# Optimization experiments

Hardware: AMD Instinct MI355X
Metric: run time of the kernel (lower is better)

The kernel has to match this reference:

```python
import jax, jax.numpy as jnp
import numpy as np

N, E, B = 50000, 500000, 64
IN_DIM, HID, H, NC = 128, 32, 8, 10
SLOPE = 0.2  # DGL GATConv leaky_relu negative_slope default


def setup_inputs() -> dict:
    key = jax.random.key(0)
    ks = jax.random.split(key, 14)
    feat = jax.random.normal(ks[0], (N, IN_DIM), dtype=jnp.float32)
    src = jax.random.randint(ks[1], (E,), 0, N, dtype=jnp.int32)
    dst = jax.random.randint(ks[2], (E,), 0, N, dtype=jnp.int32)
    node2graph = jnp.sort(jax.random.randint(ks[3], (N,), 0, B, dtype=jnp.int32))
    s1 = 1.0 / np.sqrt(IN_DIM)
    s2 = 1.0 / np.sqrt(H * HID)
    W1 = jax.random.normal(ks[4], (IN_DIM, H * HID), dtype=jnp.float32) * s1
    al1 = jax.random.normal(ks[5], (H, HID), dtype=jnp.float32) * 0.1
    ar1 = jax.random.normal(ks[6], (H, HID), dtype=jnp.float32) * 0.1
    b1 = jnp.zeros((H * HID,), dtype=jnp.float32)
    W2 = jax.random.normal(ks[7], (H * HID, H * HID), dtype=jnp.float32) * s2
    al2 = jax.random.normal(ks[8], (H, HID), dtype=jnp.float32) * 0.1
    ar2 = jax.random.normal(ks[9], (H, HID), dtype=jnp.float32) * 0.1
    b2 = jnp.zeros((H * HID,), dtype=jnp.float32)
    Wc = jax.random.normal(ks[10], (H * HID, NC), dtype=jnp.float32) * s2
    bc = jnp.zeros((NC,), dtype=jnp.float32)
    return dict(feat=feat, src=src, dst=dst, node2graph=node2graph,
                W1=W1, al1=al1, ar1=ar1, b1=b1,
                W2=W2, al2=al2, ar2=ar2, b2=b2, Wc=Wc, bc=bc)


def gat_layer(h, src, dst, W, al, ar, b):
    # h: [N, F_in] -> out: [N, H, HID]   (DGL GATConv math, no dropout)
    fs = (h @ W).reshape(N, H, HID)                      # projected src/dst feats
    el = jnp.sum(fs * al[None], axis=-1)                 # [N, H]
    er = jnp.sum(fs * ar[None], axis=-1)                 # [N, H]
    e = jax.nn.leaky_relu(el[src] + er[dst], SLOPE)      # [E, H] per-edge logits
    # edge softmax over incoming edges of each dst node (numerically stable)
    emax = jax.ops.segment_max(e, dst, num_segments=N)   # [N, H]
    ex = jnp.exp(e - emax[dst])                          # [E, H]
    denom = jax.ops.segment_sum(ex, dst, num_segments=N) # [N, H]
    alpha = ex / denom[dst]                              # [E, H]
    msg = alpha[:, :, None] * fs[src]                    # [E, H, HID]
    rst = jax.ops.segment_sum(msg, dst, num_segments=N)  # [N, H, HID]
    return rst + b.reshape(1, H, HID)


def reference(feat, src, dst, node2graph, W1, al1, ar1, b1, W2, al2, ar2, b2, Wc, bc):
    h = jax.nn.relu(gat_layer(feat, src, dst, W1, al1, ar1, b1)).reshape(N, H * HID)
    h = gat_layer(h, src, dst, W2, al2, ar2, b2).reshape(N, H * HID)
    # dgl.mean_nodes: per-graph mean over nodes of the batched graph
    counts = jax.ops.segment_sum(jnp.ones((N,), dtype=h.dtype), node2graph, num_segments=B)
    hg = jax.ops.segment_sum(h, node2graph, num_segments=B) / jnp.maximum(counts, 1.0)[:, None]
    return hg @ Wc + bc  # [B, NC]
```

## Files before the change

kernel.cpp:

```cpp
#include <hip/hip_runtime.h>
#include <hip/hip_bf16.h>

#define N_NODES 50000
#define N_EDGES 500000
#define N_GRAPHS 64
#define FDIM 256
#define NHEAD 8
#define NC 10
#define SLOPE 0.2f
#define MPAD 50048
#define NBKT 196
#define CNTN (NBKT * 256)
#define SCAN_NB (CNTN / 1024)
#define NB1 256
#define EPB 1956
#define LDSW 40
#define PSPLIT 16

typedef __attribute__((ext_vector_type(8))) short bf16x8;
typedef __attribute__((ext_vector_type(4))) float f32x4;
typedef __attribute__((ext_vector_type(2))) float f32x2;
typedef __attribute__((ext_vector_type(4))) unsigned u32x4;

__device__ __forceinline__ unsigned short f2bf(float f) {
  unsigned x = __float_as_uint(f);
  x += 0x7fff + ((x >> 16) & 1);
  return (unsigned short)(x >> 16);
}
__device__ __forceinline__ float b2f(unsigned short u) {
  return __uint_as_float((unsigned)u << 16);
}
__device__ __forceinline__ int fswz(int node, int off) {
  return off ^ ((node & 7) << 5) ^ (((node >> 3) & 1) << 4);
}

__global__ void cast_gstart_kernel(const float* __restrict__ W1, const float* __restrict__ W2,
                                   unsigned short* __restrict__ Wt1, unsigned short* __restrict__ Wt2,
                                   const int* __restrict__ n2g, int* __restrict__ gstart) {
  int e = blockIdx.x * blockDim.x + threadIdx.x;
  if (e < 256 * 128) {
    int n = e / 128, k = e % 128;
    Wt1[(size_t)n * 128 + k] = f2bf(W1[(size_t)k * 256 + n]);
  } else if (e < 256 * 128 + 256 * 256) {
    int t2 = e - 256 * 128;
    int n = t2 / 256, k = t2 % 256;
    Wt2[(size_t)n * 256 + k] = f2bf(W2[(size_t)k * 256 + n]);
  } else {
    int i = e - (256 * 128 + 256 * 256);
    if (i < N_NODES) {
      int g1 = n2g[i];
      int g0 = (i == 0) ? -1 : n2g[i - 1];
      for (int g = g0 + 1; g <= g1; ++g) gstart[g] = i;
      if (i == N_NODES - 1) {
        for (int g = g1 + 1; g <= N_GRAPHS; ++g) gstart[g] = N_NODES;
      }
    }
  }
}

__global__ void bucket_hist_kernel(const int* __restrict__ dst, int* __restrict__ counts) {
  __shared__ int hist[NBKT];
  int t = threadIdx.x, b = blockIdx.x;
  if (t < NBKT) hist[t] = 0;
  __syncthreads();
  int start = b * EPB;
  int end = min(start + EPB, N_EDGES);
  for (int base = start + t * 4; base < end; base += 1024) {
    if (base + 3 < end) {
      int4 d = *(const int4*)(dst + base);
      atomicAdd(&hist[d.x >> 8], 1); atomicAdd(&hist[d.y >> 8], 1);
      atomicAdd(&hist[d.z >> 8], 1); atomicAdd(&hist[d.w >> 8], 1);
    } else {
      for (int e2 = base; e2 < end; ++e2) atomicAdd(&hist[dst[e2] >> 8], 1);
    }
  }
  __syncthreads();
  if (t < NBKT) counts[t * NB1 + b] = hist[t];
}

__global__ void scan_local_kernel(const int* __restrict__ deg, int* __restrict__ outv,
                                  int* __restrict__ bsum, int n) {
  __shared__ int ws[4];
  int t = threadIdx.x, lane = t & 63, w = t >> 6;
  int base = blockIdx.x * 1024 + t * 4;
  int4 v = make_int4(0, 0, 0, 0);
  if (base + 3 < n) {
    v = *(const int4*)(deg + base);
  } else {
    if (base + 0 < n) v.x = deg[base + 0];
    if (base + 1 < n) v.y = deg[base + 1];
    if (base + 2 < n) v.z = deg[base + 2];
    if (base + 3 < n) v.w = deg[base + 3];
  }
  int s = v.x + v.y + v.z + v.w;
  int x = s;
  #pragma unroll
  for (int off = 1; off < 64; off <<= 1) {
    int y = __shfl_up(x, off);
    if (lane >= off) x += y;
  }
  if (lane == 63) ws[w] = x;
  __syncthreads();
  int woff = 0;
  #pragma unroll
  for (int i = 0; i < 4; ++i) woff += (i < w) ? ws[i] : 0;
  int excl = woff + x - s;
  int4 o;
  o.x = excl;
  o.y = excl + v.x;
  o.z = excl + v.x + v.y;
  o.w = excl + v.x + v.y + v.z;
  if (base + 3 < n) {
    *(int4*)(outv + base) = o;
  } else {
    if (base + 0 < n) outv[base + 0] = o.x;
    if (base + 1 < n) outv[base + 1] = o.y;
    if (base + 2 < n) outv[base + 2] = o.z;
    if (base + 3 < n) outv[base + 3] = o.w;
  }
  if (t == 255) bsum[blockIdx.x] = woff + x;
}

__global__ void scan_add_kernel(int* __restrict__ cbase, const int* __restrict__ bsum,
                                int* __restrict__ rowstart, int n) {
  __shared__ int boff[64];
  int t = threadIdx.x;
  if (t < 64) {
    int v = (t < SCAN_NB) ? bsum[t] : 0;
    int x = v;
    #pragma unroll
    for (int off = 1; off < 64; off <<= 1) {
      int y = __shfl_up(x, off);
      if (t >= off) x += y;
    }
    boff[t] = x - v;
  }
  __syncthreads();
  int i = blockIdx.x * blockDim.x + threadIdx.x;
  if (i < n) cbase[i] += boff[i >> 10];
  if (i == 0) rowstart[N_NODES] = N_EDGES;
}

__global__ void bucket_scatter_kernel(const int* __restrict__ src, const int* __restrict__ dst,
                                      const int* __restrict__ cbase, int2* __restrict__ ebuf) {
  __shared__ int cur[NBKT];
  int t = threadIdx.x, b = blockIdx.x;
  if (t < NBKT) cur[t] = 0;
  __syncthreads();
  int start = b * EPB;
  int end = min(start + EPB, N_EDGES);
  for (int base = start + t * 4; base < end; base += 1024) {
    if (base + 3 < end) {
      int4 s = *(const int4*)(src + base);
      int4 d = *(const int4*)(dst + base);
      int bk, r;
      bk = d.x >> 8; r = atomicAdd(&cur[bk], 1); ebuf[cbase[bk * NB1 + b] + r] = make_int2(s.x, d.x);
      bk = d.y >> 8; r = atomicAdd(&cur[bk], 1); ebuf[cbase[bk * NB1 + b] + r] = make_int2(s.y, d.y);
      bk = d.z >> 8; r = atomicAdd(&cur[bk], 1); ebuf[cbase[bk * NB1 + b] + r] = make_int2(s.z, d.z);
      bk = d.w >> 8; r = atomicAdd(&cur[bk], 1); ebuf[cbase[bk * NB1 + b] + r] = make_int2(s.w, d.w);
    } else {
      for (int e2 = base; e2 < end; ++e2) {
        int dd = dst[e2];
        int bk = dd >> 8;
        int r = atomicAdd(&cur[bk], 1);
        ebuf[cbase[bk * NB1 + b] + r] = make_int2(src[e2], dd);
      }
    }
  }
}

__global__ void csr_bucket_kernel(const int2* __restrict__ ebuf, const int* __restrict__ cbase,
                                  int* __restrict__ rowstart, int* __restrict__ esrc) {
  __shared__ int hist[256];
  __shared__ int cur[256];
  __shared__ int ws[4];
  int t = threadIdx.x;
  int bkt = blockIdx.x;
  int segstart = cbase[bkt * NB1];
  int segend = (bkt + 1 < NBKT) ? cbase[(bkt + 1) * NB1] : N_EDGES;
  hist[t] = 0;
  __syncthreads();
  for (int e = segstart + t; e < segend; e += 256)
    atomicAdd(&hist[ebuf[e].y & 255], 1);
  __syncthreads();
  int lane = t & 63, w = t >> 6;
  int v = hist[t], x = v;
  #pragma unroll
  for (int off = 1; off < 64; off <<= 1) {
    int y = __shfl_up(x, off);
    if (lane >= off) x += y;
  }
  if (lane == 63) ws[w] = x;
  __syncthreads();
  int woff = 0;
  #pragma unroll
  for (int i = 0; i < 4; ++i) woff += (i < w) ? ws[i] : 0;
  int excl = woff + x - v;
  cur[t] = excl;
  int node = bkt * 256 + t;
  if (node < N_NODES) rowstart[node] = segstart + excl;
  __syncthreads();
  for (int e = segstart + t; e < segend; e += 256) {
    int2 p = ebuf[e];
    int r = atomicAdd(&cur[p.y & 255], 1);
    esrc[segstart + r] = p.x;
  }
}

template<int K, bool AF32>
__global__ void gemm_mfma(const void* __restrict__ Avoid,
                          const unsigned short* __restrict__ Wt,
                          unsigned char* __restrict__ fs,
                          const float* __restrict__ al, const float* __restrict__ ar,
                          float* __restrict__ el, float* __restrict__ er, int nrows) {
  constexpr int KC = K / 32;
  __shared__ __align__(16) unsigned short LDSbuf[(64 + 256) * LDSW];
  unsigned short* Albs = LDSbuf;
  unsigned short* Wlds = LDSbuf + 64 * LDSW;
  const float* Af = (const float*)Avoid;
  const unsigned short* Ab = (const unsigned short*)Avoid;
  int t = threadIdx.x;
  int lane = t & 63;
  int w = t >> 6;
  int row0 = blockIdx.x * 64;
  int m = lane & 15;
  int q = lane >> 4;
  float4 a32[2];
  bf16x8 a16;
  bf16x8 wtr[4];
  int arow = t >> 2, apiece = t & 3;
  int agrow = min(row0 + arow, nrows - 1);
  int frow0 = t >> 3, fquad0 = t & 7;
  int frow1 = (256 + t) >> 3, fquad1 = t & 7;
  int fgrow0 = min(row0 + frow0, nrows - 1);
  int fgrow1 = min(row0 + frow1, nrows - 1);

  auto stage = [&](int kc) {
    if (AF32) {
      a32[0] = *(const float4*)(Af + (size_t)fgrow0 * K + kc * 32 + fquad0 * 4);
      a32[1] = *(const float4*)(Af + (size_t)fgrow1 * K + kc * 32 + fquad1 * 4);
    } else {
      a16 = *(const bf16x8*)(Ab + (size_t)agrow * K + kc * 32 + apiece * 8);
    }
    #pragma unroll
    for (int j = 0; j < 4; ++j) {
      int row = j * 64 + (t >> 2);
      wtr[j] = *(const bf16x8*)(Wt + (size_t)row * K + kc * 32 + (t & 3) * 8);
    }
  };
  auto commit = [&]() {
    if (AF32) {
      ushort4 o0, o1;
      o0.x = f2bf(a32[0].x); o0.y = f2bf(a32[0].y); o0.z = f2bf(a32[0].z); o0.w = f2bf(a32[0].w);
      o1.x = f2bf(a32[1].x); o1.y = f2bf(a32[1].y); o1.z = f2bf(a32[1].z); o1.w = f2bf(a32[1].w);
      *(ushort4*)(Albs + frow0 * LDSW + fquad0 * 4) = o0;
      *(ushort4*)(Albs + frow1 * LDSW + fquad1 * 4) = o1;
    } else {
      *(bf16x8*)(Albs + arow * LDSW + apiece * 8) = a16;
    }
    #pragma unroll
    for (int j = 0; j < 4; ++j) {
      int row = j * 64 + (t >> 2);
      *(bf16x8*)(Wlds + row * LDSW + (t & 3) * 8) = wtr[j];
    }
  };

  f32x4 acc[16];
  #pragma unroll
  for (int nt = 0; nt < 16; ++nt) acc[nt] = (f32x4){0.f, 0.f, 0.f, 0.f};

  stage(0);
  commit();
  for (int kc = 0; kc < KC; ++kc) {
    __syncthreads();
    if (kc + 1 < KC) stage(kc + 1);
    bf16x8 af = *(const bf16x8*)(Albs + (w * 16 + m) * LDSW + q * 8);
    #pragma unroll
    for (int nt = 0; nt < 16; ++nt) {
      bf16x8 bfv = *(const bf16x8*)(Wlds + (nt * 16 + m) * LDSW + q * 8);
      acc[nt] = __builtin_amdgcn_mfma_f32_16x16x32_bf16(bfv, af, acc[nt], 0, 0, 0);
    }
    __syncthreads();
    if (kc + 1 < KC) commit();
  }
  unsigned char* fsst = (unsigned char*)LDSbuf;
  float* elst = (float*)(fsst + 16384);
  float* erst = elst + 512;

  int nloc = w * 16 + m;
  float elh[NHEAD], erh[NHEAD];
  #pragma unroll
  for (int h = 0; h < NHEAD; ++h) { elh[h] = 0.f; erh[h] = 0.f; }
  #pragma unroll
  for (int nt = 0; nt < 16; ++nt) {
    int h = nt >> 1;
    int c0 = (nt & 1) * 16 + q * 4;
    float4 a4 = *(const float4*)(al + h * 32 + c0);
    float4 r4 = *(const float4*)(ar + h * 32 + c0);
    elh[h] += acc[nt][0] * a4.x + acc[nt][1] * a4.y + acc[nt][2] * a4.z + acc[nt][3] * a4.w;
    erh[h] += acc[nt][0] * r4.x + acc[nt][1] * r4.y + acc[nt][2] * r4.z + acc[nt][3] * r4.w;
  }
  #pragma unroll
  for (int h = 0; h < NHEAD; ++h) {
    elh[h] += __shfl_xor(elh[h], 16); elh[h] += __shfl_xor(elh[h], 32);
    erh[h] += __shfl_xor(erh[h], 16); erh[h] += __shfl_xor(erh[h], 32);
  }
  #pragma unroll
  for (int nt = 0; nt < 16; ++nt) {
    int pk = 0;
    pk = __builtin_amdgcn_cvt_pk_fp8_f32(acc[nt][0], acc[nt][1], pk, false);
    pk = __builtin_amdgcn_cvt_pk_fp8_f32(acc[nt][2], acc[nt][3], pk, true);
    *(unsigned*)(fsst + nloc * 256 + fswz(nloc, nt * 16 + q * 4)) = (unsigned)pk;
  }
  *(float2*)(elst + nloc * 8 + q * 2) = make_float2(elh[2 * q], elh[2 * q + 1]);
  *(float2*)(erst + nloc * 8 + q * 2) = make_float2(erh[2 * q], erh[2 * q + 1]);
  __syncthreads();
  #pragma unroll
  for (int i = 0; i < 4; ++i) {
    int p = i * 4096 + t * 16;
    int nn = p >> 8, off = p & 255;
    u32x4 d = *(const u32x4*)(fsst + nn * 256 + fswz(nn, off));
    *(u32x4*)(fs + (size_t)row0 * 256 + p) = d;
  }
  if (t < 128) {
    *(float4*)(el + (size_t)row0 * 8 + t * 4) = *(const float4*)(elst + t * 4);
  } else {
    int tt = t - 128;
    *(float4*)(er + (size_t)row0 * 8 + tt * 4) = *(const float4*)(erst + tt * 4);
  }
}

template<bool RELU>
__global__ __launch_bounds__(256, 8)
void edge_agg_kernel(const int* __restrict__ rowstart, const int* __restrict__ esrc,
                     const float* __restrict__ el, const float* __restrict__ er,
                     const unsigned char* __restrict__ fs,
                     const float* __restrict__ bias,
                     unsigned short* __restrict__ out, int nnodes) {
  int gid = blockIdx.x * blockDim.x + threadIdx.x;
  int v = gid >> 6;
  int lane = threadIdx.x & 63;
  if (v >= nnodes) return;
  int h = lane >> 3;
  int t8 = lane >> 3;
  int hh = lane & 7;
  int row0 = rowstart[v];
  int deg = rowstart[v + 1] - row0;
  float er_w = er[v * NHEAD + hh];
  const unsigned char* fsl = fs + lane * 4;
  const float* elp = el;
  float4 acc0 = make_float4(0.f, 0.f, 0.f, 0.f);
  float4 acc1 = make_float4(0.f, 0.f, 0.f, 0.f);
  float ws0 = 0.f, ws1 = 0.f;
  for (int base = 0; base < deg; base += 64) {
    int mm = min(deg - base, 64);
    int li = (lane < mm) ? lane : (mm - 1);
    int es = esrc[row0 + base + li];
    for (int j0 = 0; j0 < mm; j0 += 8) {
      int sj = __shfl(es, min(j0 + t8, mm - 1));
      float x = elp[(unsigned)sj * 8u + hh] + er_w;
      x = fmaxf(x, SLOPE * x);
      float wp = __expf(x);
      if (j0 + t8 >= mm) wp = 0.f;
      float wt[8]; unsigned f[8];
      #pragma unroll
      for (int t = 0; t < 8; ++t) wt[t] = __shfl(wp, t * 8 + h);
      #pragma unroll
      for (int t = 0; t < 8; ++t) {
        int s = __shfl(es, min(j0 + t, mm - 1));
        f[t] = *(const unsigned*)(fsl + ((unsigned)s << 8));
      }
      #pragma unroll
      for (int t = 0; t < 8; ++t) {
        float wgt = wt[t];
        f32x2 lo = __builtin_amdgcn_cvt_pk_f32_fp8(f[t], false);
        f32x2 hi = __builtin_amdgcn_cvt_pk_f32_fp8(f[t], true);
        if (t & 1) {
          ws1 += wgt;
          acc1.x = fmaf(wgt, lo.x, acc1.x);
          acc1.y = fmaf(wgt, lo.y, acc1.y);
          acc1.z = fmaf(wgt, hi.x, acc1.z);
          acc1.w = fmaf(wgt, hi.y, acc1.w);
        } else {
          ws0 += wgt;
          acc0.x = fmaf(wgt, lo.x, acc0.x);
          acc0.y = fmaf(wgt, lo.y, acc0.y);
          acc0.z = fmaf(wgt, hi.x, acc0.z);
          acc0.w = fmaf(wgt, hi.y, acc0.w);
        }
      }
    }
  }
  float wsum = ws0 + ws1;
  float4 acc;
  acc.x = acc0.x + acc1.x; acc.y = acc0.y + acc1.y;
  acc.z = acc0.z + acc1.z; acc.w = acc0.w + acc1.w;
  float rdenom = (deg > 0) ? (1.0f / wsum) : 0.f;
  const float4 b = *(const float4*)(bias + lane * 4);
  acc.x = fmaf(acc.x, rdenom, b.x);
  acc.y = fmaf(acc.y, rdenom, b.y);
  acc.z = fmaf(acc.z, rdenom, b.z);
  acc.w = fmaf(acc.w, rdenom, b.w);
  if (RELU) {
    acc.x = fmaxf(acc.x, 0.f); acc.y = fmaxf(acc.y, 0.f);
    acc.z = fmaxf(acc.z, 0.f); acc.w = fmaxf(acc.w, 0.f);
  }
  ushort4 o;
  o.x = f2bf(acc.x); o.y = f2bf(acc.y); o.z = f2bf(acc.z); o.w = f2bf(acc.w);
  *(ushort4*)(out + (size_t)v * FDIM + lane * 4) = o;
}

__global__ void pool_partial_kernel(const unsigned short* __restrict__ h2,
                                    const int* __restrict__ gstart,
                                    float* __restrict__ ppart) {
  int t = threadIdx.x;
  int g = blockIdx.x / PSPLIT;
  int s = blockIdx.x % PSPLIT;
  int n0 = gstart[g], n1 = gstart[g + 1];
  int cnt = n1 - n0;
  int chunk = (cnt + PSPLIT - 1) / PSPLIT;
  int a = n0 + s * chunk;
  int b = min(a + chunk, n1);
  float s0 = 0.f, s1 = 0.f, s2 = 0.f, s3 = 0.f;
  int n = a;
  for (; n + 4 <= b; n += 4) {
    s0 += b2f(h2[(size_t)(n + 0) * FDIM + t]);
    s1 += b2f(h2[(size_t)(n + 1) * FDIM + t]);
    s2 += b2f(h2[(size_t)(n + 2) * FDIM + t]);
    s3 += b2f(h2[(size_t)(n + 3) * FDIM + t]);
  }
  for (; n < b; ++n) s0 += b2f(h2[(size_t)n * FDIM + t]);
  ppart[(size_t)blockIdx.x * FDIM + t] = (s0 + s1) + (s2 + s3);
}

__global__ void pool_reduce_kernel(const float* __restrict__ ppart, float* __restrict__ hg) {
  int t = threadIdx.x;
  int g = blockIdx.x;
  float s = 0.f;
  #pragma unroll
  for (int sp = 0; sp < PSPLIT; ++sp)
    s += ppart[(size_t)(g * PSPLIT + sp) * FDIM + t];
  hg[(size_t)g * FDIM + t] = s;
}

__global__ void classifier_kernel(const float* __restrict__ hgsum, const int* __restrict__ gstart,
                                  const float* __restrict__ Wc, const float* __restrict__ bcv,
                                  float* __restrict__ out) {
  int tid = blockIdx.x * blockDim.x + threadIdx.x;
  if (tid >= N_GRAPHS * NC) return;
  int b = tid / NC, j = tid % NC;
  int cnt = gstart[b + 1] - gstart[b];
  float inv = (cnt > 0) ? (1.0f / (float)cnt) : 1.0f;
  float s = 0.f;
  for (int c = 0; c < FDIM; ++c) s += hgsum[b * FDIM + c] * Wc[c * NC + j];
  out[tid] = s * inv + bcv[j];
}

extern "C" void kernel_launch(void* const* d_in, const int* in_sizes, int n_in,
                              void* d_out, int out_size, void* d_ws, size_t ws_size,
                              hipStream_t stream) {
  const float* feat = (const float*)d_in[0];
  const int* src    = (const int*)d_in[1];
  const int* dst    = (const int*)d_in[2];
  const int* n2g    = (const int*)d_in[3];
  const float* W1  = (const float*)d_in[4];
  const float* al1 = (const float*)d_in[5];
  const float* ar1 = (const float*)d_in[6];
  const float* b1  = (const float*)d_in[7];
  const float* W2  = (const float*)d_in[8];
  const float* al2 = (const float*)d_in[9];
  const float* ar2 = (const float*)d_in[10];
  const float* b2  = (const float*)d_in[11];
  const float* Wc  = (const float*)d_in[12];
  const float* bc  = (const float*)d_in[13];
  float* out = (float*)d_out;

  char* wp = (char*)d_ws;
  auto carve = [&](size_t bytes) -> void* {
    void* p = (void*)wp;
    wp += (bytes + 255) & ~(size_t)255;
    return p;
  };
  unsigned char* fs = (unsigned char*)carve((size_t)MPAD * FDIM);
  unsigned short* h1 = (unsigned short*)carve((size_t)MPAD * FDIM * 2);
  unsigned short* h2 = h1;
  unsigned short* Wt1 = (unsigned short*)carve((size_t)256 * 128 * 2);
  unsigned short* Wt2 = (unsigned short*)carve((size_t)256 * 256 * 2);
  float* el      = (float*)carve((size_t)MPAD * NHEAD * 4);
  float* er      = (float*)carve((size_t)MPAD * NHEAD * 4);
  int* rowstart  = (int*)  carve((size_t)(N_NODES + 1) * 4);
  int* esrc      = (int*)  carve((size_t)N_EDGES * 4);
  int* gstart    = (int*)  carve((size_t)(N_GRAPHS + 1) * 4);
  int* bsum      = (int*)  carve((size_t)SCAN_NB * 4);
  int* counts    = (int*)  carve((size_t)CNTN * 4);
  int* cbase     = (int*)  carve((size_t)CNTN * 4);
  int2* ebuf     = (int2*) carve((size_t)N_EDGES * 8);
  float* ppart   = (float*)carve((size_t)N_GRAPHS * PSPLIT * FDIM * 4);
  float* hg      = (float*)carve((size_t)N_GRAPHS * FDIM * 4);
  (void)ws_size; (void)n_in; (void)in_sizes; (void)out_size;

  cast_gstart_kernel<<<(256 * 128 + 256 * 256 + N_NODES + 255) / 256, 256, 0, stream>>>(
      W1, W2, Wt1, Wt2, n2g, gstart);

  bucket_hist_kernel<<<NB1, 256, 0, stream>>>(dst, counts);
  scan_local_kernel<<<SCAN_NB, 256, 0, stream>>>(counts, cbase, bsum, CNTN);
  scan_add_kernel<<<(CNTN + 255) / 256, 256, 0, stream>>>(cbase, bsum, rowstart, CNTN);
  bucket_scatter_kernel<<<NB1, 256, 0, stream>>>(src, dst, cbase, ebuf);
  csr_bucket_kernel<<<NBKT, 256, 0, stream>>>(ebuf, cbase, rowstart, esrc);

  gemm_mfma<128, true><<<MPAD / 64, 256, 0, stream>>>(
      (const void*)feat, Wt1, fs, al1, ar1, el, er, N_NODES);
  edge_agg_kernel<true><<<(N_NODES * 64 + 255) / 256, 256, 0, stream>>>(
      rowstart, esrc, el, er, fs, b1, h1, N_NODES);

  gemm_mfma<256, false><<<MPAD / 64, 256, 0, stream>>>(
      (const void*)h1, Wt2, fs, al2, ar2, el, er, N_NODES);
  edge_agg_kernel<false><<<(N_NODES * 64 + 255) / 256, 256, 0, stream>>>(
      rowstart, esrc, el, er, fs, b2, h2, N_NODES);

  pool_partial_kernel<<<N_GRAPHS * PSPLIT, 256, 0, stream>>>(h2, gstart, ppart);
  pool_reduce_kernel<<<N_GRAPHS, 256, 0, stream>>>(ppart, hg);
  classifier_kernel<<<(N_GRAPHS * NC + 255) / 256, 256, 0, stream>>>(hg, gstart, Wc, bc, out);
}
```

Before: 229.7 us.

## Fuse preprocessing and pooling kernels, software-pipeline edge aggregation across four nodes

Merges the weight-cast and bucket-histogram kernels into one launch, and folds the scan-add step into the scatter and CSR kernels, which now rebuild the block offsets locally. The pool reduction and classifier are fused into one kernel that uses a wave-level shuffle reduction. The edge aggregation kernel now has each wave process four destination nodes and prefetches the next group of neighbour features and logits while the current group is accumulated, with launch bounds lowered to 6 blocks. The aim is fewer launches and more latency hiding on the gather loads, at the cost of more registers and a separate slow path for nodes with degree above 64.

```diff
diff --git a/kernel.cpp b/kernel.cpp
--- a/kernel.cpp
+++ b/kernel.cpp
@@ -16,6 +16,8 @@
 #define EPB 1956
 #define LDSW 40
 #define PSPLIT 16
+#define CAST_THREADS (256*128 + 256*256 + N_NODES)
+#define CAST_NB ((CAST_THREADS + 255) / 256)
 
 typedef __attribute__((ext_vector_type(8))) short bf16x8;
 typedef __attribute__((ext_vector_type(4))) float f32x4;
@@ -34,10 +36,34 @@
   return off ^ ((node & 7) << 5) ^ (((node >> 3) & 1) << 4);
 }
 
-__global__ void cast_gstart_kernel(const float* __restrict__ W1, const float* __restrict__ W2,
-                                   unsigned short* __restrict__ Wt1, unsigned short* __restrict__ Wt2,
-                                   const int* __restrict__ n2g, int* __restrict__ gstart) {
-  int e = blockIdx.x * blockDim.x + threadIdx.x;
+__global__ void cast_hist_kernel(const float* __restrict__ W1, const float* __restrict__ W2,
+                                 unsigned short* __restrict__ Wt1, unsigned short* __restrict__ Wt2,
+                                 const int* __restrict__ n2g, int* __restrict__ gstart,
+                                 const int* __restrict__ dst, int* __restrict__ counts,
+                                 int* __restrict__ rowstart) {
+  int t = threadIdx.x;
+  if (blockIdx.x < NB1) {
+    __shared__ int hist[NBKT];
+    int b = blockIdx.x;
+    if (t < NBKT) hist[t] = 0;
+    __syncthreads();
+    int start = b * EPB;
+    int end = min(start + EPB, N_EDGES);
+    for (int base = start + t * 4; base < end; base += 1024) {
+      if (base + 3 < end) {
+        int4 d = *(const int4*)(dst + base);
+        atomicAdd(&hist[d.x >> 8], 1); atomicAdd(&hist[d.y >> 8], 1);
+        atomicAdd(&hist[d.z >> 8], 1); atomicAdd(&hist[d.w >> 8], 1);
+      } else {
+        for (int e2 = base; e2 < end; ++e2) atomicAdd(&hist[dst[e2] >> 8], 1);
+      }
+    }
+    __syncthreads();
+    if (t < NBKT) counts[t * NB1 + b] = hist[t];
+    return;
+  }
+  int e = (blockIdx.x - NB1) * 256 + t;
+  if (e == 0) rowstart[N_NODES] = N_EDGES;
   if (e < 256 * 128) {
     int n = e / 128, k = e % 128;
     Wt1[(size_t)n * 128 + k] = f2bf(W1[(size_t)k * 256 + n]);
@@ -58,26 +84,6 @@
   }
 }
 
-__global__ void bucket_hist_kernel(const int* __restrict__ dst, int* __restrict__ counts) {
-  __shared__ int hist[NBKT];
-  int t = threadIdx.x, b = blockIdx.x;
-  if (t < NBKT) hist[t] = 0;
-  __syncthreads();
-  int start = b * EPB;
-  int end = min(start + EPB, N_EDGES);
-  for (int base = start + t * 4; base < end; base += 1024) {
-    if (base + 3 < end) {
-      int4 d = *(const int4*)(dst + base);
-      atomicAdd(&hist[d.x >> 8], 1); atomicAdd(&hist[d.y >> 8], 1);
-      atomicAdd(&hist[d.z >> 8], 1); atomicAdd(&hist[d.w >> 8], 1);
-    } else {
-      for (int e2 = base; e2 < end; ++e2) atomicAdd(&hist[dst[e2] >> 8], 1);
-    }
-  }
-  __syncthreads();
-  if (t < NBKT) counts[t * NB1 + b] = hist[t];
-}
-
 __global__ void scan_local_kernel(const int* __restrict__ deg, int* __restrict__ outv,
                                   int* __restrict__ bsum, int n) {
   __shared__ int ws[4];
@@ -121,10 +127,12 @@
   if (t == 255) bsum[blockIdx.x] = woff + x;
 }
 
-__global__ void scan_add_kernel(int* __restrict__ cbase, const int* __restrict__ bsum,
-                                int* __restrict__ rowstart, int n) {
-  __shared__ int boff[64];
-  int t = threadIdx.x;
+__global__ void bucket_scatter_kernel(const int* __restrict__ src, const int* __restrict__ dst,
+                                      const int* __restrict__ cbase, const int* __restrict__ bsum,
+                                      int2* __restrict__ ebuf) {
+  __shared__ int cur[NBKT];
+  __shared__ int boffl[SCAN_NB];
+  int t = threadIdx.x, b = blockIdx.x;
   if (t < 64) {
     int v = (t < SCAN_NB) ? bsum[t] : 0;
     int x = v;
@@ -133,19 +141,13 @@
       int y = __shfl_up(x, off);
       if (t >= off) x += y;
     }
-    boff[t] = x - v;
-  }
-  __syncthreads();
-  int i = blockIdx.x * blockDim.x + threadIdx.x;
-  if (i < n) cbase[i] += boff[i >> 10];
-  if (i == 0) rowstart[N_NODES] = N_EDGES;
-}
-
-__global__ void bucket_scatter_kernel(const int* __restrict__ src, const int* __restrict__ dst,
-                                      const int* __restrict__ cbase, int2* __restrict__ ebuf) {
-  __shared__ int cur[NBKT];
-  int t = threadIdx.x, b = blockIdx.x;
-  if (t < NBKT) cur[t] = 0;
+    if (t < SCAN_NB) boffl[t] = x - v;
+  }
+  __syncthreads();
+  if (t < NBKT) {
+    int idx = t * NB1 + b;
+    cur[t] = cbase[idx] + boffl[idx >> 10];
+  }
   __syncthreads();
   int start = b * EPB;
   int end = min(start + EPB, N_EDGES);
@@ -153,33 +155,50 @@
     if (base + 3 < end) {
       int4 s = *(const int4*)(src + base);
       int4 d = *(const int4*)(dst + base);
-      int bk, r;
-      bk = d.x >> 8; r = atomicAdd(&cur[bk], 1); ebuf[cbase[bk * NB1 + b] + r] = make_int2(s.x, d.x);
-      bk = d.y >> 8; r = atomicAdd(&cur[bk], 1); ebuf[cbase[bk * NB1 + b] + r] = make_int2(s.y, d.y);
-      bk = d.z >> 8; r = atomicAdd(&cur[bk], 1); ebuf[cbase[bk * NB1 + b] + r] = make_int2(s.z, d.z);
-      bk = d.w >> 8; r = atomicAdd(&cur[bk], 1); ebuf[cbase[bk * NB1 + b] + r] = make_int2(s.w, d.w);
+      int r;
+      r = atomicAdd(&cur[d.x >> 8], 1); ebuf[r] = make_int2(s.x, d.x);
+      r = atomicAdd(&cur[d.y >> 8], 1); ebuf[r] = make_int2(s.y, d.y);
+      r = atomicAdd(&cur[d.z >> 8], 1); ebuf[r] = make_int2(s.z, d.z);
+      r = atomicAdd(&cur[d.w >> 8], 1); ebuf[r] = make_int2(s.w, d.w);
     } else {
       for (int e2 = base; e2 < end; ++e2) {
         int dd = dst[e2];
-        int bk = dd >> 8;
-        int r = atomicAdd(&cur[bk], 1);
-        ebuf[cbase[bk * NB1 + b] + r] = make_int2(src[e2], dd);
+        int r = atomicAdd(&cur[dd >> 8], 1);
+        ebuf[r] = make_int2(src[e2], dd);
       }
     }
   }
 }
 
 __global__ void csr_bucket_kernel(const int2* __restrict__ ebuf, const int* __restrict__ cbase,
+                                  const int* __restrict__ bsum,
                                   int* __restrict__ rowstart, int* __restrict__ esrc) {
   __shared__ int hist[256];
   __shared__ int cur[256];
   __shared__ int ws[4];
+  __shared__ int boffl[SCAN_NB];
   int t = threadIdx.x;
   int bkt = blockIdx.x;
-  int segstart = cbase[bkt * NB1];
-  int segend = (bkt + 1 < NBKT) ? cbase[(bkt + 1) * NB1] : N_EDGES;
   hist[t] = 0;
-  __syncthreads();
+  if (t >= 64 && t < 128) {
+    int tt = t - 64;
+    int v = (tt < SCAN_NB) ? bsum[tt] : 0;
+    int x = v;
+    #pragma unroll
+    for (int off = 1; off < 64; off <<= 1) {
+      int y = __shfl_up(x, off);
+      if (tt >= off) x += y;
+    }
+    if (tt < SCAN_NB) boffl[tt] = x - v;
+  }
+  __syncthreads();
+  int i0 = bkt * NB1;
+  int segstart = cbase[i0] + boffl[i0 >> 10];
+  int segend = N_EDGES;
+  if (bkt + 1 < NBKT) {
+    int i1 = (bkt + 1) * NB1;
+    segend = cbase[i1] + boffl[i1 >> 10];
+  }
   for (int e = segstart + t; e < segend; e += 256)
     atomicAdd(&hist[ebuf[e].y & 255], 1);
   __syncthreads();
@@ -331,50 +350,80 @@
 }
 
 template<bool RELU>
-__global__ __launch_bounds__(256, 8)
+__global__ __launch_bounds__(256, 6)
 void edge_agg_kernel(const int* __restrict__ rowstart, const int* __restrict__ esrc,
                      const float* __restrict__ el, const float* __restrict__ er,
                      const unsigned char* __restrict__ fs,
                      const float* __restrict__ bias,
                      unsigned short* __restrict__ out, int nnodes) {
-  int gid = blockIdx.x * blockDim.x + threadIdx.x;
-  int v = gid >> 6;
   int lane = threadIdx.x & 63;
-  if (v >= nnodes) return;
+  int w = threadIdx.x >> 6;
+  int v0 = (blockIdx.x * 4 + w) * 4;
+  if (v0 >= nnodes) return;
   int h = lane >> 3;
   int t8 = lane >> 3;
   int hh = lane & 7;
-  int row0 = rowstart[v];
-  int deg = rowstart[v + 1] - row0;
-  float er_w = er[v * NHEAD + hh];
   const unsigned char* fsl = fs + lane * 4;
   const float* elp = el;
-  float4 acc0 = make_float4(0.f, 0.f, 0.f, 0.f);
-  float4 acc1 = make_float4(0.f, 0.f, 0.f, 0.f);
-  float ws0 = 0.f, ws1 = 0.f;
-  for (int base = 0; base < deg; base += 64) {
-    int mm = min(deg - base, 64);
-    int li = (lane < mm) ? lane : (mm - 1);
-    int es = esrc[row0 + base + li];
-    for (int j0 = 0; j0 < mm; j0 += 8) {
-      int sj = __shfl(es, min(j0 + t8, mm - 1));
-      float x = elp[(unsigned)sj * 8u + hh] + er_w;
-      x = fmaxf(x, SLOPE * x);
-      float wp = __expf(x);
-      if (j0 + t8 >= mm) wp = 0.f;
-      float wt[8]; unsigned f[8];
+  const float4 b = *(const float4*)(bias + lane * 4);
+
+  int rsl = rowstart[min(v0 + lane, nnodes)];
+  int rs[5];
+  #pragma unroll
+  for (int i = 0; i < 5; ++i) rs[i] = __shfl(rsl, i);
+  int degv[4], mmx[4], es[4];
+  float erw[4];
+  #pragma unroll
+  for (int i = 0; i < 4; ++i) {
+    degv[i] = rs[i + 1] - rs[i];
+    mmx[i] = min(degv[i], 64);
+    erw[i] = er[(unsigned)(v0 + i) * 8u + hh];
+    es[i] = 0;
+    if (mmx[i] > 0) es[i] = esrc[rs[i] + min(lane, mmx[i] - 1)];
+  }
+
+  auto issue = [&](int esv, int mmv, float erv, int gbase, float& x, unsigned* f) {
+    int sj = __shfl(esv, max(min(gbase + t8, mmv - 1), 0));
+    x = elp[(unsigned)sj * 8u + hh] + erv;
+    #pragma unroll
+    for (int t = 0; t < 8; ++t) {
+      int s = __shfl(esv, max(min(gbase + t, mmv - 1), 0));
+      f[t] = *(const unsigned*)(fsl + ((unsigned)s << 8));
+    }
+  };
+
+  float xC; unsigned fC[8];
+  issue(es[0], mmx[0], erw[0], 0, xC, fC);
+
+  #pragma unroll
+  for (int i = 0; i < 4; ++i) {
+    float4 acc0 = make_float4(0.f, 0.f, 0.f, 0.f);
+    float4 acc1 = make_float4(0.f, 0.f, 0.f, 0.f);
+    float ws0 = 0.f, ws1 = 0.f;
+    int G = max((mmx[i] + 7) >> 3, 1);
+    for (int g = 0; g < G; ++g) {
+      bool last = (g + 1 >= G);
+      float xN = 0.f; unsigned fN[8];
+      #pragma unroll
+      for (int t = 0; t < 8; ++t) fN[t] = 0u;
+      if (!(last && i == 3)) {
+        int esn = last ? es[(i < 3) ? i + 1 : 3] : es[i];
+        int mmn = last ? mmx[(i < 3) ? i + 1 : 3] : mmx[i];
+        float ern = last ? erw[(i < 3) ? i + 1 : 3] : erw[i];
+        int gbn = last ? 0 : (g + 1) * 8;
+        issue(esn, mmn, ern, gbn, xN, fN);
+      }
+      float xl = fmaxf(xC, SLOPE * xC);
+      float wp = __expf(xl);
+      if (g * 8 + t8 >= mmx[i]) wp = 0.f;
+      float wt[8];
       #pragma unroll
       for (int t = 0; t < 8; ++t) wt[t] = __shfl(wp, t * 8 + h);
       #pragma unroll
       for (int t = 0; t < 8; ++t) {
-        int s = __shfl(es, min(j0 + t, mm - 1));
-        f[t] = *(const unsigned*)(fsl + ((unsigned)s << 8));
-      }
-      #pragma unroll
-      for (int t = 0; t < 8; ++t) {
         float wgt = wt[t];
-        f32x2 lo = __builtin_amdgcn_cvt_pk_f32_fp8(f[t], false);
-        f32x2 hi = __builtin_amdgcn_cvt_pk_f32_fp8(f[t], true);
+        f32x2 lo = __builtin_amdgcn_cvt_pk_f32_fp8(fC[t], false);
+        f32x2 hi = __builtin_amdgcn_cvt_pk_f32_fp8(fC[t], true);
         if (t & 1) {
           ws1 += wgt;
           acc1.x = fmaf(wgt, lo.x, acc1.x);
@@ -389,25 +438,63 @@
           acc0.w = fmaf(wgt, hi.y, acc0.w);
         }
       }
-    }
-  }
-  float wsum = ws0 + ws1;
-  float4 acc;
-  acc.x = acc0.x + acc1.x; acc.y = acc0.y + acc1.y;
-  acc.z = acc0.z + acc1.z; acc.w = acc0.w + acc1.w;
-  float rdenom = (deg > 0) ? (1.0f / wsum) : 0.f;
-  const float4 b = *(const float4*)(bias + lane * 4);
-  acc.x = fmaf(acc.x, rdenom, b.x);
-  acc.y = fmaf(acc.y, rdenom, b.y);
-  acc.z = fmaf(acc.z, rdenom, b.z);
-  acc.w = fmaf(acc.w, rdenom, b.w);
-  if (RELU) {
-    acc.x = fmaxf(acc.x, 0.f); acc.y = fmaxf(acc.y, 0.f);
-    acc.z = fmaxf(acc.z, 0.f); acc.w = fmaxf(acc.w, 0.f);
-  }
-  ushort4 o;
-  o.x = f2bf(acc.x); o.y = f2bf(acc.y); o.z = f2bf(acc.z); o.w = f2bf(acc.w);
-  *(ushort4*)(out + (size_t)v * FDIM + lane * 4) = o;
+      xC = xN;
+      #pragma unroll
+      for (int t = 0; t < 8; ++t) fC[t] = fN[t];
+    }
+    if (__builtin_expect(degv[i] > 64, 0)) {
+      for (int base = 64; base < degv[i]; base += 64) {
+        int mm2 = min(degv[i] - base, 64);
+        int es2 = esrc[rs[i] + base + min(lane, mm2 - 1)];
+        for (int j0 = 0; j0 < mm2; j0 += 8) {
+          int sj = __shfl(es2, min(j0 + t8, mm2 - 1));
+          float x = elp[(unsigned)sj * 8u + hh] + erw[i];
+          x = fmaxf(x, SLOPE * x);
+          float wp2 = __expf(x);
+          if (j0 + t8 >= mm2) wp2 = 0.f;
+          float wt[8]; unsigned f2[8];
+          #pragma unroll
+          for (int t = 0; t < 8; ++t) wt[t] = __shfl(wp2, t * 8 + h);
+          #pragma unroll
+          for (int t = 0; t < 8; ++t) {
+            int s = __shfl(es2, min(j0 + t, mm2 - 1));
+            f2[t] = *(const unsigned*)(fsl + ((unsigned)s << 8));
+          }
+          #pragma unroll
+          for (int t = 0; t < 8; ++t) {
+            float wgt = wt[t];
+            f32x2 lo = __builtin_amdgcn_cvt_pk_f32_fp8(f2[t], false);
+            f32x2 hi = __builtin_amdgcn_cvt_pk_f32_fp8(f2[t], true);
+            if (t & 1) {
+              ws1 += wgt;
+              acc1.x = fmaf(wgt, lo.x, acc1.x); acc1.y = fmaf(wgt, lo.y, acc1.y);
+              acc1.z = fmaf(wgt, hi.x, acc1.z); acc1.w = fmaf(wgt, hi.y, acc1.w);
+            } else {
+              ws0 += wgt;
+              acc0.x = fmaf(wgt, lo.x, acc0.x); acc0.y = fmaf(wgt, lo.y, acc0.y);
+              acc0.z = fmaf(wgt, hi.x, acc0.z); acc0.w = fmaf(wgt, hi.y, acc0.w);
+            }
+          }
+        }
+      }
+    }
+    float wsum = ws0 + ws1;
+    float4 acc;
+    acc.x = acc0.x + acc1.x; acc.y = acc0.y + acc1.y;
+    acc.z = acc0.z + acc1.z; acc.w = acc0.w + acc1.w;
+    float rdenom = (degv[i] > 0) ? (1.0f / wsum) : 0.f;
+    acc.x = fmaf(acc.x, rdenom, b.x);
+    acc.y = fmaf(acc.y, rdenom, b.y);
+    acc.z = fmaf(acc.z, rdenom, b.z);
+    acc.w = fmaf(acc.w, rdenom, b.w);
+    if (RELU) {
+      acc.x = fmaxf(acc.x, 0.f); acc.y = fmaxf(acc.y, 0.f);
+      acc.z = fmaxf(acc.z, 0.f); acc.w = fmaxf(acc.w, 0.f);
+    }
+    ushort4 o;
+    o.x = f2bf(acc.x); o.y = f2bf(acc.y); o.z = f2bf(acc.z); o.w = f2bf(acc.w);
+    *(ushort4*)(out + (size_t)(v0 + i) * FDIM + lane * 4) = o;
+  }
 }
 
 __global__ void pool_partial_kernel(const unsigned short* __restrict__ h2,
@@ -420,40 +507,44 @@
   int cnt = n1 - n0;
   int chunk = (cnt + PSPLIT - 1) / PSPLIT;
   int a = n0 + s * chunk;
-  int b = min(a + chunk, n1);
+  int bnd = min(a + chunk, n1);
   float s0 = 0.f, s1 = 0.f, s2 = 0.f, s3 = 0.f;
   int n = a;
-  for (; n + 4 <= b; n += 4) {
+  for (; n + 4 <= bnd; n += 4) {
     s0 += b2f(h2[(size_t)(n + 0) * FDIM + t]);
     s1 += b2f(h2[(size_t)(n + 1) * FDIM + t]);
     s2 += b2f(h2[(size_t)(n + 2) * FDIM + t]);
     s3 += b2f(h2[(size_t)(n + 3) * FDIM + t]);
   }
-  for (; n < b; ++n) s0 += b2f(h2[(size_t)n * FDIM + t]);
+  for (; n < bnd; ++n) s0 += b2f(h2[(size_t)n * FDIM + t]);
   ppart[(size_t)blockIdx.x * FDIM + t] = (s0 + s1) + (s2 + s3);
 }
 
-__global__ void pool_reduce_kernel(const float* __restrict__ ppart, float* __restrict__ hg) {
-  int t = threadIdx.x;
-  int g = blockIdx.x;
+__global__ void pool_cls_kernel(const float* __restrict__ ppart, const int* __restrict__ gstart,
+                                const float* __restrict__ Wc, const float* __restrict__ bcv,
+                                float* __restrict__ out) {
+  __shared__ float hgl[FDIM];
+  int t = threadIdx.x, g = blockIdx.x;
   float s = 0.f;
   #pragma unroll
   for (int sp = 0; sp < PSPLIT; ++sp)
     s += ppart[(size_t)(g * PSPLIT + sp) * FDIM + t];
-  hg[(size_t)g * FDIM + t] = s;
-}
-
-__global__ void classifier_kernel(const float* __restrict__ hgsum, const int* __restrict__ gstart,
-                                  const float* __restrict__ Wc, const float* __restrict__ bcv,
-                                  float* __restrict__ out) {
-  int tid = blockIdx.x * blockDim.x + threadIdx.x;
-  if (tid >= N_GRAPHS * NC) return;
-  int b = tid / NC, j = tid % NC;
-  int cnt = gstart[b + 1] - gstart[b];
+  hgl[t] = s;
+  __syncthreads();
+  int cnt = gstart[g + 1] - gstart[g];
   float inv = (cnt > 0) ? (1.0f / (float)cnt) : 1.0f;
-  float s = 0.f;
-  for (int c = 0; c < FDIM; ++c) s += hgsum[b * FDIM + c] * Wc[c * NC + j];
-  out[tid] = s * inv + bcv[j];
+  int w = t >> 6, lane = t & 63;
+  for (int j = w; j < NC; j += 4) {
+    float p = 0.f;
+    #pragma unroll
+    for (int k = 0; k < 4; ++k) {
+      int c = lane * 4 + k;
+      p += hgl[c] * Wc[c * NC + j];
+    }
+    #pragma unroll
+    for (int off = 1; off < 64; off <<= 1) p += __shfl_xor(p, off);
+    if (lane == 0) out[g * NC + j] = p * inv + bcv[j];
+  }
 }
 
 extern "C" void kernel_launch(void* const* d_in, const int* in_sizes, int n_in,
@@ -496,29 +587,24 @@
   int* cbase     = (int*)  carve((size_t)CNTN * 4);
   int2* ebuf     = (int2*) carve((size_t)N_EDGES * 8);
   float* ppart   = (float*)carve((size_t)N_GRAPHS * PSPLIT * FDIM * 4);
-  float* hg      = (float*)carve((size_t)N_GRAPHS * FDIM * 4);
   (void)ws_size; (void)n_in; (void)in_sizes; (void)out_size;
 
-  cast_gstart_kernel<<<(256 * 128 + 256 * 256 + N_NODES + 255) / 256, 256, 0, stream>>>(
-      W1, W2, Wt1, Wt2, n2g, gstart);
-
-  bucket_hist_kernel<<<NB1, 256, 0, stream>>>(dst, counts);
+  cast_hist_kernel<<<NB1 + CAST_NB, 256, 0, stream>>>(
+      W1, W2, Wt1, Wt2, n2g, gstart, dst, counts, rowstart);
   scan_local_kernel<<<SCAN_NB, 256, 0, stream>>>(counts, cbase, bsum, CNTN);
-  scan_add_kernel<<<(CNTN + 255) / 256, 256, 0, stream>>>(cbase, bsum, rowstart, CNTN);
-  bucket_scatter_kernel<<<NB1, 256, 0, stream>>>(src, dst, cbase, ebuf);
-  csr_bucket_kernel<<<NBKT, 256, 0, stream>>>(ebuf, cbase, rowstart, esrc);
+  bucket_scatter_kernel<<<NB1, 256, 0, stream>>>(src, dst, cbase, bsum, ebuf);
+  csr_bucket_kernel<<<NBKT, 256, 0, stream>>>(ebuf, cbase, bsum, rowstart, esrc);
 
   gemm_mfma<128, true><<<MPAD / 64, 256, 0, stream>>>(
       (const void*)feat, Wt1, fs, al1, ar1, el, er, N_NODES);
-  edge_agg_kernel<true><<<(N_NODES * 64 + 255) / 256, 256, 0, stream>>>(
+  edge_agg_kernel<true><<<(N_NODES + 15) / 16, 256, 0, stream>>>(
       rowstart, esrc, el, er, fs, b1, h1, N_NODES);
 
   gemm_mfma<256, false><<<MPAD / 64, 256, 0, stream>>>(
       (const void*)h1, Wt2, fs, al2, ar2, el, er, N_NODES);
-  edge_agg_kernel<false><<<(N_NODES * 64 + 255) / 256, 256, 0, stream>>>(
+  edge_agg_kernel<false><<<(N_NODES + 15) / 16, 256, 0, stream>>>(
       rowstart, esrc, el, er, fs, b2, h2, N_NODES);
 
   pool_partial_kernel<<<N_GRAPHS * PSPLIT, 256, 0, stream>>>(h2, gstart, ppart);
-  pool_reduce_kernel<<<N_GRAPHS, 256, 0, stream>>>(ppart, hg);
-  classifier_kernel<<<(N_GRAPHS * NC + 255) / 256, 256, 0, stream>>>(hg, gstart, Wc, bc, out);
-}
+  pool_cls_kernel<<<N_GRAPHS, 256, 0, stream>>>(ppart, gstart, Wc, bc, out);
+}
```

Measured after the change: 254.7 us. +10.9%, slower.
